# Optimization experiments

Measured on AMD Instinct MI355X. Metric: run time of the kernel, lower is better.

Reference implementation:

```python
import jax, jax.numpy as jnp
import numpy as np

CODEBOOK_SIZE = 8192
DIM = 256
COMMITMENT_COST = 0.25


def setup_inputs() -> dict:
    key = jax.random.key(0)
    k1, k2 = jax.random.split(key)
    z = jax.random.normal(k1, (8, DIM, 1024), dtype=jnp.float32)
    # nn.init.uniform_(codebook.weight, -1/K, 1/K)
    bound = 1.0 / CODEBOOK_SIZE
    codebook = jax.random.uniform(k2, (CODEBOOK_SIZE, DIM), dtype=jnp.float32,
                                  minval=-bound, maxval=bound)
    return {"z": z, "codebook": codebook}


def reference(z, codebook):
    B, D, T = z.shape
    z_perm = jnp.transpose(z, (0, 2, 1)).reshape(B * T, D)  # (BT, D)
    # ||z||^2 - 2 z.c + ||c||^2  -> (BT, K)
    distances = (jnp.sum(z_perm * z_perm, axis=1, keepdims=True)
                 - 2.0 * (z_perm @ codebook.T)
                 + jnp.sum(codebook * codebook, axis=1)[None, :])
    indices = jnp.argmin(distances, axis=1)          # (BT,)
    z_q_flat = codebook[indices]                     # (BT, D)
    z_q = jnp.transpose(z_q_flat.reshape(B, T, D), (0, 2, 1))  # (B, D, T)

    codebook_loss = jnp.mean((z_q - jax.lax.stop_gradient(z)) ** 2)
    commitment_loss = COMMITMENT_COST * jnp.mean((jax.lax.stop_gradient(z_q) - z) ** 2)
    loss = codebook_loss + commitment_loss

    # straight-through estimator
    z_q_st = z + jax.lax.stop_gradient(z_q - z)
    return z_q_st, indices.reshape(B, T), loss
```

## Files before the change

### kernel.cpp

```cpp
#include <hip/hip_runtime.h>

#define DD   256
#define TT   1024
#define BT   8192
#define KK   8192
#define ZQ_SIZE 2097152

#define FLT_INF 3.402823466e38f

typedef __attribute__((ext_vector_type(8))) short short8;
typedef __attribute__((ext_vector_type(4))) float f32x4;

#define A2_B    0u
#define B2_B    12582912u
#define AN_B    25165824u
#define CN_B    25198592u
#define KEY_B   25231360u
#define ACC_B   25296896u

static __device__ __forceinline__ unsigned short f2bf(float x) {
    unsigned int u = __float_as_uint(x);
    return (unsigned short)((u + 0x7FFF + ((u >> 16) & 1)) >> 16);
}
static __device__ __forceinline__ float bf2f(unsigned short h) {
    return __uint_as_float(((unsigned int)h) << 16);
}
static __device__ __forceinline__ void split3(float x, unsigned short& h,
                                              unsigned short& m, unsigned short& l) {
    h = f2bf(x);
    float r1 = x - bf2f(h);
    m = f2bf(r1);
    l = f2bf(r1 - bf2f(m));
}

static __device__ __forceinline__ void gld16(const void* g, const void* l) {
    __builtin_amdgcn_global_load_lds(
        (const __attribute__((address_space(1))) unsigned int*)g,
        (__attribute__((address_space(3))) unsigned int*)l, 16, 0, 0);
}

__global__ __launch_bounds__(256) void vq_prep(const float* __restrict__ z,
                                               const float* __restrict__ cb,
                                               float* __restrict__ An,
                                               unsigned short* __restrict__ A2,
                                               unsigned short* __restrict__ B2,
                                               float* __restrict__ Cn,
                                               unsigned long long* __restrict__ keys,
                                               float* __restrict__ lacc) {
    __shared__ float T[64][257];
    int tid = threadIdx.x;
    if (blockIdx.x < 2048) {
        int g = blockIdx.x * 256 + tid;
        int code = g >> 6, d4 = (g & 63) * 4;
        if (d4 == 0) {
            keys[code] = ~0ull;
            if (code == 0) *lacc = 0.f;
        }
        float4 v = *(const float4*)&cb[(size_t)code * DD + d4];
        unsigned short h[4], m[4], l[4];
        split3(v.x, h[0], m[0], l[0]);
        split3(v.y, h[1], m[1], l[1]);
        split3(v.z, h[2], m[2], l[2]);
        split3(v.w, h[3], m[3], l[3]);
        int ng = code >> 4;
        int lane = ((d4 >> 3) & 3) * 16 + (code & 15);
        int kk = d4 >> 5;
        int jb = d4 & 7;
        size_t base = (size_t)((ng * 3) * 8 + kk) * 512 + lane * 8 + jb;
        *(ushort4*)&B2[base]        = make_ushort4(h[0], h[1], h[2], h[3]);
        *(ushort4*)&B2[base + 4096] = make_ushort4(m[0], m[1], m[2], m[3]);
        *(ushort4*)&B2[base + 8192] = make_ushort4(l[0], l[1], l[2], l[3]);
        float s = v.x * v.x + v.y * v.y + v.z * v.z + v.w * v.w;
        #pragma unroll
        for (int off = 32; off; off >>= 1) s += __shfl_down(s, off, 64);
        if ((tid & 63) == 0) Cn[code] = s;
    } else {
        int blk = blockIdx.x - 2048;
        int b = blk >> 4;
        int t0 = (blk & 15) * 64;
        #pragma unroll
        for (int it = 0; it < 16; ++it) {
            int d = it * 16 + (tid >> 4);
            int t4 = (tid & 15) * 4;
            float4 v = *(const float4*)&z[(size_t)b * (DD * TT) + (size_t)d * TT + t0 + t4];
            T[t4 + 0][d] = v.x; T[t4 + 1][d] = v.y; T[t4 + 2][d] = v.z; T[t4 + 3][d] = v.w;
        }
        __syncthreads();
        int r = tid >> 2, q = tid & 3;
        int t = b * 1024 + t0 + r;
        int gA = t >> 4, ml = t & 15;
        float s = 0.f;
        #pragma unroll
        for (int dd = 0; dd < 16; ++dd) {
            int d = dd * 16 + q * 4;
            float v0 = T[r][d], v1 = T[r][d + 1], v2 = T[r][d + 2], v3 = T[r][d + 3];
            unsigned short h[4], m[4], l[4];
            split3(v0, h[0], m[0], l[0]);
            split3(v1, h[1], m[1], l[1]);
            split3(v2, h[2], m[2], l[2]);
            split3(v3, h[3], m[3], l[3]);
            s = s + v0 * v0; s = s + v1 * v1; s = s + v2 * v2; s = s + v3 * v3;
            int kk = d >> 5, quad = (d >> 3) & 3, jb = d & 7;
            size_t base = (size_t)((gA * 3) * 8 + kk) * 512 + (quad * 16 + ml) * 8 + jb;
            *(ushort4*)&A2[base]        = make_ushort4(h[0], h[1], h[2], h[3]);
            *(ushort4*)&A2[base + 4096] = make_ushort4(m[0], m[1], m[2], m[3]);
            *(ushort4*)&A2[base + 8192] = make_ushort4(l[0], l[1], l[2], l[3]);
        }
        s += __shfl_down(s, 1, 4);
        s += __shfl_down(s, 2, 4);
        if (q == 0) An[t] = s;
    }
}

__global__ __launch_bounds__(256, 2) void vq_scores(const unsigned short* __restrict__ A2,
                                                    const unsigned short* __restrict__ B2,
                                                    const float* __restrict__ An,
                                                    const float* __restrict__ Cn,
                                                    unsigned long long* __restrict__ keys) {
    __shared__ __attribute__((aligned(16))) unsigned short Bl[2][12288];

    int bid = blockIdx.x;
    int g = bid >> 6, sl = bid & 63;
    int mt = (g >> 3) * 8 + (sl >> 3);
    int nt = (g & 7) * 8 + (sl & 7);
    const int token0 = mt * 256, code0 = nt * 128;

    const int wid = threadIdx.x >> 6, lane = threadIdx.x & 63;
    const int quad = lane >> 4, col = lane & 15;

    int sidx[6]; size_t soff[6];
    #pragma unroll
    for (int n = 0; n < 6; ++n) {
        int idx = wid * 6 + n;
        int p = idx >> 3, ngl = idx & 7;
        sidx[n] = idx * 512;
        soff[n] = (size_t)(((nt * 8 + ngl) * 3 + p) * 8) * 512 + lane * 8;
    }

    f32x4 acc[4][8];
    #pragma unroll
    for (int i = 0; i < 4; ++i)
        #pragma unroll
        for (int j = 0; j < 8; ++j) acc[i][j] = (f32x4){0.f, 0.f, 0.f, 0.f};

    #pragma unroll
    for (int n = 0; n < 6; ++n)
        gld16(B2 + soff[n], &Bl[0][sidx[n]]);

    const int gm0 = (token0 >> 4) + wid * 4;
    const int PP[6] = {2, 1, 1, 0, 0, 0};
    const int QQ[6] = {0, 0, 1, 1, 2, 0};

    for (int kk = 0; kk < 8; ++kk) {
        __syncthreads();
        if (kk < 7) {
            #pragma unroll
            for (int n = 0; n < 6; ++n)
                gld16(B2 + soff[n] + (size_t)(kk + 1) * 512, &Bl[(kk + 1) & 1][sidx[n]]);
        }
        const unsigned short* B = Bl[kk & 1];
        short8 af[4], bf[8];
        #pragma unroll
        for (int t = 0; t < 6; ++t) {
            const int p = PP[t], q = QQ[t];
            if (t == 0 || p != PP[t - 1]) {
                #pragma unroll
                for (int i = 0; i < 4; ++i)
                    af[i] = *(const short8*)&A2[(size_t)(((gm0 + i) * 3 + p) * 8 + kk) * 512
                                                + lane * 8];
            }
            if (t == 0 || q != QQ[t - 1]) {
                #pragma unroll
                for (int j = 0; j < 8; ++j)
                    bf[j] = *(const short8*)&B[(q * 8 + j) * 512 + lane * 8];
            }
            #pragma unroll
            for (int i = 0; i < 4; ++i)
                #pragma unroll
                for (int j = 0; j < 8; ++j)
                    acc[i][j] = __builtin_amdgcn_mfma_f32_16x16x32_bf16(
                        af[i], bf[j], acc[i][j], 0, 0, 0);
        }
    }

    float cn[8]; int cidx[8];
    #pragma unroll
    for (int j = 0; j < 8; ++j) {
        cidx[j] = code0 + j * 16 + col;
        cn[j] = Cn[cidx[j]];
    }
    #pragma unroll
    for (int i = 0; i < 4; ++i) {
        #pragma unroll
        for (int r = 0; r < 4; ++r) {
            int token = token0 + wid * 64 + i * 16 + quad * 4 + r;
            float Ai = An[token];
            float bv = FLT_INF; int bi = 0;
            #pragma unroll
            for (int j = 0; j < 8; ++j) {
                float d1 = fmaf(-2.f, acc[i][j][r], Ai);
                float dist = d1 + cn[j];
                if (dist < bv) { bv = dist; bi = cidx[j]; }
            }
            #pragma unroll
            for (int off = 8; off; off >>= 1) {
                float ov = __shfl_down(bv, off, 16);
                int   oi = __shfl_down(bi, off, 16);
                if (ov < bv || (ov == bv && oi < bi)) { bv = ov; bi = oi; }
            }
            if (col == 0) {
                unsigned long long key =
                    ((unsigned long long)__float_as_uint(bv) << 32) | (unsigned)bi;
                atomicMin(&keys[token], key);
            }
        }
    }
}

__global__ __launch_bounds__(256) void vq_gather(const float* __restrict__ z,
                                                 const float* __restrict__ cb,
                                                 const unsigned long long* __restrict__ keys,
                                                 float* __restrict__ out,
                                                 float* __restrict__ out_idx,
                                                 float* __restrict__ loss_acc) {
    int e4 = blockIdx.x * 256 + threadIdx.x;
    int t4 = e4 & 255;
    int rest = e4 >> 8;
    int d = rest & 255;
    int b = rest >> 8;
    int gbase = b * 1024 + t4 * 4;

    const int* klo = (const int*)keys;
    int i0 = klo[(size_t)(gbase + 0) * 2];
    int i1 = klo[(size_t)(gbase + 1) * 2];
    int i2 = klo[(size_t)(gbase + 2) * 2];
    int i3 = klo[(size_t)(gbase + 3) * 2];
    if (d == 0) {
        out_idx[gbase + 0] = (float)i0;
        out_idx[gbase + 1] = (float)i1;
        out_idx[gbase + 2] = (float)i2;
        out_idx[gbase + 3] = (float)i3;
    }

    float4 zv = *(const float4*)&z[(size_t)e4 * 4];
    float q0 = cb[(size_t)i0 * DD + d];
    float q1 = cb[(size_t)i1 * DD + d];
    float q2 = cb[(size_t)i2 * DD + d];
    float q3 = cb[(size_t)i3 * DD + d];

    float d0 = q0 - zv.x, d1 = q1 - zv.y, d2 = q2 - zv.z, d3 = q3 - zv.w;
    float4 o;
    o.x = zv.x + d0; o.y = zv.y + d1; o.z = zv.z + d2; o.w = zv.w + d3;
    *(float4*)&out[(size_t)e4 * 4] = o;

    float s = d0 * d0 + d1 * d1 + d2 * d2 + d3 * d3;
    #pragma unroll
    for (int off = 32; off; off >>= 1) s += __shfl_down(s, off, 64);
    __shared__ float wsum[4];
    if ((threadIdx.x & 63) == 0) wsum[threadIdx.x >> 6] = s;
    __syncthreads();
    if (threadIdx.x == 0)
        atomicAdd(loss_acc, wsum[0] + wsum[1] + wsum[2] + wsum[3]);
}

__global__ void vq_loss(const float* __restrict__ loss_acc, float* __restrict__ out_loss) {
    *out_loss = 1.25f * (*loss_acc) / 2097152.f;
}

extern "C" void kernel_launch(void* const* d_in, const int* in_sizes, int n_in,
                              void* d_out, int out_size, void* d_ws, size_t ws_size,
                              hipStream_t stream) {
    const float* z  = (const float*)d_in[0];
    const float* cb = (const float*)d_in[1];
    float* out = (float*)d_out;
    char*  w   = (char*)d_ws;

    unsigned short* A2 = (unsigned short*)(w + A2_B);
    unsigned short* B2 = (unsigned short*)(w + B2_B);
    float* An = (float*)(w + AN_B);
    float* Cn = (float*)(w + CN_B);
    unsigned long long* keys = (unsigned long long*)(w + KEY_B);
    float* lacc = (float*)(w + ACC_B);

    vq_prep   <<<2048 + 128, 256, 0, stream>>>(z, cb, An, A2, B2, Cn, keys, lacc);
    vq_scores <<<2048, 256, 0, stream>>>(A2, B2, An, Cn, keys);
    vq_gather <<<ZQ_SIZE / 1024, 256, 0, stream>>>(z, cb, keys, out, out + ZQ_SIZE, lacc);
    vq_loss   <<<1, 1, 0, stream>>>(lacc, out + ZQ_SIZE + BT);
}
```

Measured before the change: 277.0 us.

## Load codebook fragments directly from global memory instead of LDS double-buffering

Removes the shared-memory double buffer for the codebook tiles, which were filled asynchronously with global_load_lds, along with the per-k-step __syncthreads. Both A and B fragments are now read straight from global memory, relying on L2/L1 cache for reuse across waves. The precision-term order is changed so the B fragments stay resident while A fragments are reloaded for every term. This frees LDS and removes barriers, but it increases global and cache traffic and adds load latency that is no longer hidden by prefetching.

Result: slower. 294.1 us (+6.2%).

```diff
diff --git a/kernel.cpp b/kernel.cpp
--- a/kernel.cpp
+++ b/kernel.cpp
@@ -31,12 +31,6 @@
     float r1 = x - bf2f(h);
     m = f2bf(r1);
     l = f2bf(r1 - bf2f(m));
-}
-
-static __device__ __forceinline__ void gld16(const void* g, const void* l) {
-    __builtin_amdgcn_global_load_lds(
-        (const __attribute__((address_space(1))) unsigned int*)g,
-        (__attribute__((address_space(3))) unsigned int*)l, 16, 0, 0);
 }
 
 __global__ __launch_bounds__(256) void vq_prep(const float* __restrict__ z,
@@ -117,8 +111,6 @@
                                                     const float* __restrict__ An,
                                                     const float* __restrict__ Cn,
                                                     unsigned long long* __restrict__ keys) {
-    __shared__ __attribute__((aligned(16))) unsigned short Bl[2][12288];
-
     int bid = blockIdx.x;
     int g = bid >> 6, sl = bid & 63;
     int mt = (g >> 3) * 8 + (sl >> 3);
@@ -128,52 +120,33 @@
     const int wid = threadIdx.x >> 6, lane = threadIdx.x & 63;
     const int quad = lane >> 4, col = lane & 15;
 
-    int sidx[6]; size_t soff[6];
-    #pragma unroll
-    for (int n = 0; n < 6; ++n) {
-        int idx = wid * 6 + n;
-        int p = idx >> 3, ngl = idx & 7;
-        sidx[n] = idx * 512;
-        soff[n] = (size_t)(((nt * 8 + ngl) * 3 + p) * 8) * 512 + lane * 8;
-    }
-
     f32x4 acc[4][8];
     #pragma unroll
     for (int i = 0; i < 4; ++i)
         #pragma unroll
         for (int j = 0; j < 8; ++j) acc[i][j] = (f32x4){0.f, 0.f, 0.f, 0.f};
 
-    #pragma unroll
-    for (int n = 0; n < 6; ++n)
-        gld16(B2 + soff[n], &Bl[0][sidx[n]]);
-
     const int gm0 = (token0 >> 4) + wid * 4;
-    const int PP[6] = {2, 1, 1, 0, 0, 0};
-    const int QQ[6] = {0, 0, 1, 1, 2, 0};
+    const int ngb = nt * 8;
+    const int PP[6] = {0, 1, 2, 0, 1, 0};
+    const int QQ[6] = {0, 0, 0, 1, 1, 2};
 
     for (int kk = 0; kk < 8; ++kk) {
-        __syncthreads();
-        if (kk < 7) {
-            #pragma unroll
-            for (int n = 0; n < 6; ++n)
-                gld16(B2 + soff[n] + (size_t)(kk + 1) * 512, &Bl[(kk + 1) & 1][sidx[n]]);
-        }
-        const unsigned short* B = Bl[kk & 1];
-        short8 af[4], bf[8];
+        short8 bf[8];
         #pragma unroll
         for (int t = 0; t < 6; ++t) {
             const int p = PP[t], q = QQ[t];
-            if (t == 0 || p != PP[t - 1]) {
-                #pragma unroll
-                for (int i = 0; i < 4; ++i)
-                    af[i] = *(const short8*)&A2[(size_t)(((gm0 + i) * 3 + p) * 8 + kk) * 512
-                                                + lane * 8];
-            }
             if (t == 0 || q != QQ[t - 1]) {
                 #pragma unroll
                 for (int j = 0; j < 8; ++j)
-                    bf[j] = *(const short8*)&B[(q * 8 + j) * 512 + lane * 8];
-            }
+                    bf[j] = *(const short8*)&B2[(size_t)(((ngb + j) * 3 + q) * 8 + kk) * 512
+                                                + lane * 8];
+            }
+            short8 af[4];
+            #pragma unroll
+            for (int i = 0; i < 4; ++i)
+                af[i] = *(const short8*)&A2[(size_t)(((gm0 + i) * 3 + p) * 8 + kk) * 512
+                                            + lane * 8];
             #pragma unroll
             for (int i = 0; i < 4; ++i)
                 #pragma unroll
```
